# Kernel optimization log

Hardware: AMD Instinct MI355X
Metric: run time of the kernel (lower is better)

The kernel has to match this reference:

```python
import jax, jax.numpy as jnp
import numpy as np
import math

ANCHOR_SIZES = (128.0, 256.0, 512.0)
ANCHOR_RATIOS = (0.5, 1.0, 2.0)
NMS_THRESH = 0.7
PRE_NMS_TOPK = 6000   # rpn_test_prenms_topk (module is in eval at __init__)
POST_NMS_TOPK = 300   # rpn_test_topk
MIN_SIZE = 16.0
BBOX_CLIP = math.log(1000.0 / 16.0)


def _base_anchors():
    scales = jnp.array(ANCHOR_SIZES, jnp.float32)
    ratios = jnp.array(ANCHOR_RATIOS, jnp.float32)
    h_r = jnp.sqrt(ratios)
    w_r = 1.0 / h_r
    ws = (w_r[:, None] * scales[None, :]).reshape(-1)  # [A], ratio-major
    hs = (h_r[:, None] * scales[None, :]).reshape(-1)
    return jnp.stack([-ws, -hs, ws, hs], axis=1) * 0.5  # [A,4] centered at origin


def _grid_anchors(img_hw, feat_hw):
    Hi, Wi = img_hw
    Hf, Wf = feat_hw
    sy, sx = Hi // Hf, Wi // Wf  # feature stride
    shift_x = jnp.arange(Wf, dtype=jnp.float32) * sx
    shift_y = jnp.arange(Hf, dtype=jnp.float32) * sy
    yy, xx = jnp.meshgrid(shift_y, shift_x, indexing='ij')
    shifts = jnp.stack([xx, yy, xx, yy], axis=-1).reshape(-1, 1, 4)
    # layout (H, W, A) matches permute(0,2,3,1) flattening of the heads
    return (shifts + _base_anchors()[None]).reshape(-1, 4)


def _conv(x, w, b, pad):
    y = jax.lax.conv_general_dilated(x, w, (1, 1), pad,
                                     dimension_numbers=('NCHW', 'OIHW', 'NCHW'))
    return y + b[None, :, None, None]


def _decode(deltas, anchors):
    wa = anchors[:, 2] - anchors[:, 0]
    ha = anchors[:, 3] - anchors[:, 1]
    cxa = anchors[:, 0] + 0.5 * wa
    cya = anchors[:, 1] + 0.5 * ha
    dx, dy = deltas[:, 0], deltas[:, 1]
    dw = jnp.minimum(deltas[:, 2], BBOX_CLIP)
    dh = jnp.minimum(deltas[:, 3], BBOX_CLIP)
    cx = dx * wa + cxa
    cy = dy * ha + cya
    w = jnp.exp(dw) * wa
    h = jnp.exp(dh) * ha
    return jnp.stack([cx - 0.5 * w, cy - 0.5 * h, cx + 0.5 * w, cy + 0.5 * h], axis=1)


def _pairwise_iou(a, b):
    area_a = (a[:, 2] - a[:, 0]) * (a[:, 3] - a[:, 1])
    area_b = (b[:, 2] - b[:, 0]) * (b[:, 3] - b[:, 1])
    lt = jnp.maximum(a[:, None, :2], b[None, :, :2])
    rb = jnp.minimum(a[:, None, 2:], b[None, :, 2:])
    wh = jnp.clip(rb - lt, 0.0)
    inter = wh[..., 0] * wh[..., 1]
    return inter / (area_a[:, None] + area_b[None, :] - inter)


def _nms_keep(boxes, valid, thresh):
    # boxes are already sorted by descending score; greedy suppression
    N = boxes.shape[0]
    iou = _pairwise_iou(boxes, boxes)  # [N,N]
    idx = jnp.arange(N)

    def body(i, keep):
        sup = keep[i] & (iou[i] > thresh) & (idx > i)
        return keep & jnp.logical_not(sup)

    return jax.lax.fori_loop(0, N, body, valid)


def setup_inputs() -> dict:
    key = jax.random.key(0)
    ks = jax.random.split(key, 6)
    C, Hf, Wf = 1024, 100, 100
    Hi, Wi = 1600, 1600
    A = len(ANCHOR_SIZES) * len(ANCHOR_RATIOS)  # 9
    std = 0.01  # matches torch.nn.init.normal_(std=0.01), bias=0
    return {
        'input_image': jax.random.normal(ks[0], (1, 3, Hi, Wi), jnp.float32),
        'feature_map': jax.random.normal(ks[1], (1, C, Hf, Wf), jnp.float32),
        'conv_w': jax.random.normal(ks[2], (C, C, 3, 3), jnp.float32) * std,
        'conv_b': jnp.zeros((C,), jnp.float32),
        'obj_w': jax.random.normal(ks[3], (A, C, 1, 1), jnp.float32) * std,
        'obj_b': jnp.zeros((A,), jnp.float32),
        'reg_w': jax.random.normal(ks[4], (4 * A, C, 1, 1), jnp.float32) * std,
        'reg_b': jnp.zeros((4 * A,), jnp.float32),
    }


def reference(input_image, feature_map, conv_w, conv_b, obj_w, obj_b, reg_w, reg_b):
    Hi, Wi = input_image.shape[-2:]
    Hf, Wf = feature_map.shape[-2:]
    A = obj_w.shape[0]

    feats = jax.nn.relu(_conv(feature_map, conv_w, conv_b, 'SAME'))
    obj = _conv(feats, obj_w, obj_b, 'VALID')   # [N,A,Hf,Wf]
    reg = _conv(feats, reg_w, reg_b, 'VALID')   # [N,4A,Hf,Wf]

    obj_flat = jnp.transpose(obj, (0, 2, 3, 1)).reshape(-1)                 # [N*Hf*Wf*A]
    reg_flat = jnp.transpose(reg.reshape(-1, A, 4, Hf, Wf),
                             (0, 3, 4, 1, 2)).reshape(-1, 4)                # [N*Hf*Wf*A,4]

    anchors = _grid_anchors((Hi, Wi), (Hf, Wf))
    boxes = _decode(jax.lax.stop_gradient(reg_flat), anchors)
    probs = jax.nn.sigmoid(jax.lax.stop_gradient(obj_flat))

    k = min(PRE_NMS_TOPK, probs.shape[0])
    top_p, top_i = jax.lax.top_k(probs, k)
    b = boxes[top_i]
    b = jnp.stack([jnp.clip(b[:, 0], 0.0, Wi), jnp.clip(b[:, 1], 0.0, Hi),
                   jnp.clip(b[:, 2], 0.0, Wi), jnp.clip(b[:, 3], 0.0, Hi)], axis=1)
    valid = ((b[:, 2] - b[:, 0]) >= MIN_SIZE) & ((b[:, 3] - b[:, 1]) >= MIN_SIZE)

    keep = _nms_keep(b, valid, NMS_THRESH)
    masked = jnp.where(keep, top_p, -1.0)
    final_s, fi = jax.lax.top_k(masked, POST_NMS_TOPK)
    final_b = b[fi]
    good = final_s > 0.0  # zero-pad slots beyond the NMS survivor count
    proposals = jnp.where(good[:, None], final_b, 0.0)
    scores = jnp.where(good, final_s, 0.0)
    return proposals, scores
```

## Files before the change

### kernel.cpp

```cpp
#include <hip/hip_runtime.h>
#include <stdint.h>

typedef unsigned int uint32;
typedef unsigned long long uint64;

#define NPIX      10000
#define NCH       1024
#define NANCH     90000
#define PRE_TOPK  6000
#define POST_TOPK 300
#define SORT_N    8192
#define NWORDS    94
#define SUP_ROWS  6016
#define BBOX_CLIP_F 4.135166556742356f

#define TILE_H   8
#define TILE_W   16
#define HALO_H   10
#define HALO_W   18
#define HALO_WP  20
#define CICHUNK  16
#define CO_PER_WAVE 32

__device__ __forceinline__ uint64 shfl64(uint64 v, int lane) {
    int lo = __shfl((int)(uint32)v, lane);
    int hi = __shfl((int)(uint32)(v >> 32), lane);
    return ((uint64)(uint32)hi << 32) | (uint32)lo;
}

__global__ __launch_bounds__(256) void zero_out(float* __restrict__ out, int n) {
    int i = blockIdx.x * 256 + threadIdx.x;
    if (i < n) out[i] = 0.f;
}

__global__ __launch_bounds__(256) void repack_w(const float* __restrict__ w, float* __restrict__ W2) {
    int kk = blockIdx.x;
    int tile = blockIdx.y;
    int tci = (tile & 15) << 6;
    int tco = (tile >> 4) << 6;
    __shared__ float lds[64][65];
    int t = threadIdx.x;
    int c0 = t & 63;
    int r0 = t >> 6;
#pragma unroll
    for (int r = 0; r < 16; ++r) {
        int col = r0 + (r << 2);
        int ci = tci + c0;
        int co = tco + col;
        lds[col][c0] = w[((size_t)co * 1024 + ci) * 9 + kk];
    }
    __syncthreads();
#pragma unroll
    for (int r = 0; r < 16; ++r) {
        int row = r0 + (r << 2);
        int ci = tci + row;
        int co = tco + c0;
        W2[((size_t)kk * 1024 + ci) * 1024 + co] = lds[c0][row];
    }
}

__global__ __launch_bounds__(256) void conv_sw(const float* __restrict__ fm,
        const float* __restrict__ W2, const float* __restrict__ bias,
        float* __restrict__ feats) {
    __shared__ float xt[CICHUNK][HALO_H][HALO_WP];
    const int t = threadIdx.x;
    const int lane = t & 63;
    const int wv = t >> 6;
    const int tile = blockIdx.x;
    const int tx0 = (tile % 7) * TILE_W;
    const int ty0 = (tile / 7) * TILE_H;
    const int co0 = __builtin_amdgcn_readfirstlane((blockIdx.y << 7) + (wv << 5));
    const int ly = lane >> 3, lx = lane & 7;

    float acc0[CO_PER_WAVE] = {};
    float acc1[CO_PER_WAVE] = {};

#pragma unroll 1
    for (int c0 = 0; c0 < NCH; c0 += CICHUNK) {
        __syncthreads();
        for (int i = t; i < CICHUNK * HALO_H * HALO_W; i += 256) {
            int ci = i / (HALO_H * HALO_W);
            int rem = i - ci * (HALO_H * HALO_W);
            int hy = rem / HALO_W;
            int hx = rem - hy * HALO_W;
            int gy = ty0 - 1 + hy;
            int gx = tx0 - 1 + hx;
            bool ok = (gy >= 0) & (gy < 100) & (gx >= 0) & (gx < 100);
            xt[ci][hy][hx] = ok ? fm[(size_t)(c0 + ci) * NPIX + gy * 100 + gx] : 0.f;
        }
        __syncthreads();
#pragma unroll 1
        for (int ci = 0; ci < CICHUNK; ++ci) {
#pragma unroll
            for (int kk = 0; kk < 9; ++kk) {
                const int ky = kk / 3, kx2 = kk % 3;
                float x0v = xt[ci][ly + ky][lx + kx2];
                float x1v = xt[ci][ly + ky][lx + 8 + kx2];
                const float* wp = W2 + ((((size_t)kk << 10) + (size_t)(c0 + ci)) << 10) + co0;
#pragma unroll
                for (int c = 0; c < CO_PER_WAVE; ++c) {
                    float wgt = wp[c];
                    acc0[c] = fmaf(wgt, x0v, acc0[c]);
                    acc1[c] = fmaf(wgt, x1v, acc1[c]);
                }
            }
        }
    }

    const int gy = ty0 + ly;
    const int gx0 = tx0 + lx;
    const int gx1 = tx0 + 8 + lx;
    const bool oky = gy < 100;
#pragma unroll
    for (int c = 0; c < CO_PER_WAVE; ++c) {
        float b = bias[co0 + c];
        if (oky && (gx0 < 100)) feats[(size_t)(co0 + c) * NPIX + gy * 100 + gx0] = fmaxf(acc0[c] + b, 0.f);
        if (oky && (gx1 < 100)) feats[(size_t)(co0 + c) * NPIX + gy * 100 + gx1] = fmaxf(acc1[c] + b, 0.f);
    }
}

__global__ __launch_bounds__(256) void heads(const float* __restrict__ feats,
        const float* __restrict__ objw, const float* __restrict__ objb,
        const float* __restrict__ regw, const float* __restrict__ regb,
        uint32* __restrict__ keys32, float* __restrict__ regflat) {
    int p0 = blockIdx.x << 6;
    int t = threadIdx.x;
    int pl = t & 63;
    int g = t >> 6;
    __shared__ float fts[64][65];
    __shared__ float wl[48][64];
    float acc[12] = {};
    for (int c0 = 0; c0 < 1024; c0 += 64) {
        __syncthreads();
#pragma unroll
        for (int r = 0; r < 16; ++r) {
            int cc = g + (r << 2);
            int p = p0 + pl;
            fts[cc][pl] = (p < NPIX) ? feats[(size_t)(c0 + cc) * NPIX + p] : 0.f;
        }
#pragma unroll
        for (int i = 0; i < 12; ++i) {
            int flat = (i << 8) + t;
            int o = flat >> 6;
            int cc = flat & 63;
            float v = 0.f;
            if (o < 9) v = objw[o * 1024 + c0 + cc];
            else if (o < 45) v = regw[(o - 9) * 1024 + c0 + cc];
            wl[o][cc] = v;
        }
        __syncthreads();
#pragma unroll 16
        for (int cc = 0; cc < 64; ++cc) {
            float v = fts[cc][pl];
#pragma unroll
            for (int i = 0; i < 12; ++i)
                acc[i] = fmaf(v, wl[g + (i << 2)][cc], acc[i]);
        }
    }
    int p = p0 + pl;
    if (p < NPIX) {
#pragma unroll
        for (int i = 0; i < 12; ++i) {
            int o = g + (i << 2);
            if (o < 9) {
                float logit = acc[i] + objb[o];
                float prob = 1.f / (1.f + expf(-logit));
                keys32[p * 9 + o] = 0xFFFFFFFFu - __float_as_uint(prob);
            } else if (o < 45) {
                int ch = o - 9;
                float v = acc[i] + regb[ch];
                int a = ch >> 2, d = ch & 3;
                regflat[((size_t)p * 9 + a) * 4 + d] = v;
            }
        }
    }
}

__global__ __launch_bounds__(1024) void radix_select(const uint32* __restrict__ keys, uint32* __restrict__ meta) {
    __shared__ uint32 hist[256];
    __shared__ uint32 sPrefix, sK;
    int t = threadIdx.x;
    if (t == 0) { sPrefix = 0; sK = PRE_TOPK; }
    for (int pass = 0; pass < 4; ++pass) {
        int shift = 24 - pass * 8;
        uint32 kmask = pass ? (0xFFFFFFFFu << (32 - 8 * pass)) : 0u;
        if (t < 256) hist[t] = 0;
        __syncthreads();
        uint32 pref = sPrefix;
        for (int i = t; i < NANCH; i += 1024) {
            uint32 k = keys[i];
            if ((k & kmask) == pref) atomicAdd(&hist[(k >> shift) & 255], 1u);
        }
        __syncthreads();
        if (t == 0) {
            uint32 cum = 0, K = sK;
            for (int b = 0; b < 256; ++b) {
                uint32 c = hist[b];
                if (cum + c >= K) { sPrefix = pref | ((uint32)b << shift); sK = K - cum; break; }
                cum += c;
            }
        }
        __syncthreads();
    }
    if (t == 0) meta[0] = sPrefix;
}

__global__ __launch_bounds__(256) void compact_k(const uint32* __restrict__ keys, const uint32* __restrict__ meta,
        uint32* __restrict__ cnt, uint64* __restrict__ sel) {
    int i = blockIdx.x * 256 + threadIdx.x;
    if (i >= NANCH) return;
    uint32 T = meta[0];
    uint32 k = keys[i];
    if (k <= T) {
        uint32 pos = atomicAdd(cnt, 1u);
        if (pos < SORT_N) sel[pos] = ((uint64)k << 32) | (uint32)i;
    }
}

__global__ __launch_bounds__(1024) void bitonic_sort(const uint32* __restrict__ meta, const uint64* __restrict__ sel,
        uint64* __restrict__ sorted) {
    __shared__ uint64 arr[SORT_N];
    int t = threadIdx.x;
    uint32 cnt = meta[1]; if (cnt > SORT_N) cnt = SORT_N;
    for (int i = t; i < SORT_N; i += 1024) arr[i] = (i < (int)cnt) ? sel[i] : 0xFFFFFFFFFFFFFFFFull;
    __syncthreads();
    for (unsigned k = 2; k <= SORT_N; k <<= 1) {
        for (unsigned j = k >> 1; j > 0; j >>= 1) {
#pragma unroll 1
            for (int s = 0; s < SORT_N / 1024; ++s) {
                unsigned i = s * 1024 + t;
                unsigned l = i ^ j;
                if (l > i) {
                    uint64 a = arr[i], b = arr[l];
                    bool up = ((i & k) == 0);
                    if ((a > b) == up) { arr[i] = b; arr[l] = a; }
                }
            }
            __syncthreads();
        }
    }
    for (int i = t; i < PRE_TOPK; i += 1024) sorted[i] = arr[i];
}

__global__ __launch_bounds__(256) void decode_k(const uint64* __restrict__ sorted,
        const float* __restrict__ regflat,
        float4* __restrict__ boxes, float* __restrict__ probv, uint32* __restrict__ valid) {
    int i = blockIdx.x * 256 + threadIdx.x;
    if (i >= PRE_TOPK) return;
    uint64 v = sorted[i];
    uint32 idx = (uint32)v;
    uint32 key = (uint32)(v >> 32);
    float prob = __uint_as_float(0xFFFFFFFFu - key);
    int a = idx % 9;
    int p = idx / 9;
    int y = p / 100;
    int x = p - y * 100;
    const float ratios[3] = {0.5f, 1.0f, 2.0f};
    const float scales[3] = {128.f, 256.f, 512.f};
    float ratio = ratios[a / 3];
    float scale = scales[a % 3];
    float h_r = sqrtf(ratio);
    float w_r = 1.0f / h_r;
    float wsz = w_r * scale;
    float hsz = h_r * scale;
    float sx = 16.f * (float)x;
    float sy = 16.f * (float)y;
    float ax1 = sx - wsz * 0.5f;
    float ay1 = sy - hsz * 0.5f;
    float ax2 = sx + wsz * 0.5f;
    float ay2 = sy + hsz * 0.5f;
    float wa = ax2 - ax1;
    float ha = ay2 - ay1;
    float cxa = ax1 + 0.5f * wa;
    float cya = ay1 + 0.5f * ha;
    float dx = regflat[(size_t)idx * 4 + 0];
    float dy = regflat[(size_t)idx * 4 + 1];
    float dw = fminf(regflat[(size_t)idx * 4 + 2], BBOX_CLIP_F);
    float dh = fminf(regflat[(size_t)idx * 4 + 3], BBOX_CLIP_F);
    float cx = dx * wa + cxa;
    float cy = dy * ha + cya;
    float w = expf(dw) * wa;
    float h = expf(dh) * ha;
    float x1 = cx - 0.5f * w, y1 = cy - 0.5f * h, x2 = cx + 0.5f * w, y2 = cy + 0.5f * h;
    x1 = fminf(fmaxf(x1, 0.f), 1600.f);
    y1 = fminf(fmaxf(y1, 0.f), 1600.f);
    x2 = fminf(fmaxf(x2, 0.f), 1600.f);
    y2 = fminf(fmaxf(y2, 0.f), 1600.f);
    boxes[i] = make_float4(x1, y1, x2, y2);
    probv[i] = prob;
    valid[i] = (((x2 - x1) >= 16.f) & ((y2 - y1) >= 16.f)) ? 1u : 0u;
}

__global__ __launch_bounds__(64) void nms_pairs(const float4* __restrict__ boxes, uint64* __restrict__ sup) {
    int bi = blockIdx.y, bj = blockIdx.x;
    int t = threadIdx.x;
    int i = bi * 64 + t;
    if (bj < bi) { if (i < SUP_ROWS) sup[(size_t)i * NWORDS + bj] = 0; return; }
    __shared__ float4 bx[64];
    __shared__ float ab[64];
    int j0 = bj * 64;
    float4 bb = (j0 + t < PRE_TOPK) ? boxes[j0 + t] : make_float4(0, 0, 0, 0);
    bx[t] = bb;
    ab[t] = (bb.z - bb.x) * (bb.w - bb.y);
    __syncthreads();
    uint64 bits = 0;
    if (i < PRE_TOPK) {
        float4 ba = boxes[i];
        float aa = (ba.z - ba.x) * (ba.w - ba.y);
        for (int jj = 0; jj < 64; ++jj) {
            int j = j0 + jj;
            if (j > i && j < PRE_TOPK) {
                float4 bv = bx[jj];
                float ltx = fmaxf(ba.x, bv.x);
                float lty = fmaxf(ba.y, bv.y);
                float rbx = fminf(ba.z, bv.z);
                float rby = fminf(ba.w, bv.w);
                float wv = fmaxf(rbx - ltx, 0.f);
                float hv = fmaxf(rby - lty, 0.f);
                float inter = wv * hv;
                float iou = inter / (aa + ab[jj] - inter);
                if (iou > 0.7f) bits |= (1ull << jj);
            }
        }
    }
    if (i < SUP_ROWS) sup[(size_t)i * NWORDS + bj] = bits;
}

__global__ __launch_bounds__(64) void nms_scan(const uint32* __restrict__ valid, const uint64* __restrict__ sup,
        uint32* __restrict__ keeplist, uint32* __restrict__ kcount) {
    int l = threadIdx.x;
    __shared__ uint64 srow[64][95];
    uint64 r0 = 0, r1 = 0;
    for (int b = 0; b < 64; ++b) {
        int idx = l * 64 + b;
        if (idx < PRE_TOPK && valid[idx]) r0 |= (1ull << b);
    }
    if (l < NWORDS - 64) {
        int base = (64 + l) * 64;
        for (int b = 0; b < 64; ++b) {
            int idx = base + b;
            if (idx < PRE_TOPK && valid[idx]) r1 |= (1ull << b);
        }
    }
    int outc = 0;
    bool done = false;
    for (int c = 0; c < NWORDS && !done; ++c) {
        __syncthreads();
        for (int rr = 0; rr < 64; ++rr) {
            int row = c * 64 + rr;
            srow[rr][l] = sup[(size_t)row * NWORDS + l];
            if (l < NWORDS - 64) srow[rr][64 + l] = sup[(size_t)row * NWORDS + 64 + l];
        }
        __syncthreads();
        for (int ii = 0; ii < 64; ++ii) {
            int i = c * 64 + ii;
            if (i >= PRE_TOPK) break;
            uint64 kw = (c < 64) ? shfl64(r0, c) : shfl64(r1, c - 64);
            if ((kw >> ii) & 1ull) {
                if (l == 0) keeplist[outc] = (uint32)i;
                ++outc;
                if (outc >= POST_TOPK) { done = true; break; }
                r0 &= ~srow[ii][l];
                if (l < NWORDS - 64) r1 &= ~srow[ii][64 + l];
            }
        }
    }
    if (l == 0) *kcount = (uint32)outc;
}

__global__ __launch_bounds__(512) void finalize_k(const uint32* __restrict__ keeplist, const uint32* __restrict__ kcount,
        const float4* __restrict__ boxes, const float* __restrict__ probv, float* __restrict__ out) {
    int t = threadIdx.x;
    if (t < POST_TOPK) {
        uint32 kc = *kcount;
        if (t < (int)kc) {
            int i = keeplist[t];
            float4 b = boxes[i];
            out[t * 4 + 0] = b.x; out[t * 4 + 1] = b.y; out[t * 4 + 2] = b.z; out[t * 4 + 3] = b.w;
            out[1200 + t] = probv[i];
        } else {
            out[t * 4 + 0] = 0.f; out[t * 4 + 1] = 0.f; out[t * 4 + 2] = 0.f; out[t * 4 + 3] = 0.f;
            out[1200 + t] = 0.f;
        }
    }
}

extern "C" void kernel_launch(void* const* d_in, const int* in_sizes, int n_in,
                              void* d_out, int out_size, void* d_ws, size_t ws_size,
                              hipStream_t stream) {
    const float* fm = (const float*)d_in[1];
    const float* cw = (const float*)d_in[2];
    const float* cb = (const float*)d_in[3];
    const float* ow = (const float*)d_in[4];
    const float* ob = (const float*)d_in[5];
    const float* rw = (const float*)d_in[6];
    const float* rb = (const float*)d_in[7];
    float* out = (float*)d_out;

    uint8_t* base = (uint8_t*)d_ws;
    size_t off = 0;
    auto alloc = [&](size_t bytes) -> void* {
        void* p = base + off;
        off = (off + bytes + 255) & ~(size_t)255;
        return p;
    };
    float* feats    = (float*)alloc((size_t)NCH * NPIX * 4);
    uint32* meta    = (uint32*)alloc(64);
    uint32* keepl   = (uint32*)alloc(POST_TOPK * 4);
    uint32* kcount  = (uint32*)alloc(64);
    size_t ubase = off;
    float* W2       = (float*)alloc((size_t)9 * 1024 * 1024 * 4);
    size_t endA = off;
    off = ubase;
    uint32* keys    = (uint32*)alloc((size_t)NANCH * 4);
    float* regflat  = (float*)alloc((size_t)NANCH * 4 * 4);
    uint64* sel     = (uint64*)alloc((size_t)SORT_N * 8);
    uint64* sorted  = (uint64*)alloc((size_t)PRE_TOPK * 8);
    float4* boxes   = (float4*)alloc((size_t)PRE_TOPK * 16);
    float* probv    = (float*)alloc((size_t)PRE_TOPK * 4);
    uint32* validb  = (uint32*)alloc((size_t)PRE_TOPK * 4);
    uint64* sup     = (uint64*)alloc((size_t)SUP_ROWS * NWORDS * 8);
    size_t endB = off;
    size_t needed = (endA > endB) ? endA : endB;

    if (needed > ws_size) {
        zero_out<<<(out_size + 255) / 256, 256, 0, stream>>>(out, out_size);
        return;
    }

    hipMemsetAsync(meta, 0, 64, stream);

    repack_w<<<dim3(9, 256), 256, 0, stream>>>(cw, W2);
    conv_sw<<<dim3(91, 8), 256, 0, stream>>>(fm, W2, cb, feats);
    heads<<<157, 256, 0, stream>>>(feats, ow, ob, rw, rb, keys, regflat);
    radix_select<<<1, 1024, 0, stream>>>(keys, meta);
    compact_k<<<(NANCH + 255) / 256, 256, 0, stream>>>(keys, meta, meta + 1, sel);
    bitonic_sort<<<1, 1024, 0, stream>>>(meta, sel, sorted);
    decode_k<<<(PRE_TOPK + 255) / 256, 256, 0, stream>>>(sorted, regflat, boxes, probv, validb);
    nms_pairs<<<dim3(NWORDS, NWORDS), 64, 0, stream>>>(boxes, sup);
    nms_scan<<<1, 64, 0, stream>>>(validb, sup, keepl, kcount);
    finalize_k<<<1, 512, 0, stream>>>(keepl, kcount, boxes, probv, out);
}
```

Baseline: 3.707 ms.

## Repack conv weights per 16-channel tile and halve output channels per wave

Replaces the [kk][ci][co] weight repack with a [co-tile][ci][kk][16] layout, so each wave reads one contiguous 576-byte block of weights per input channel instead of nine strided 128-byte rows. Each wave now computes 16 output channels instead of 32, and the grid doubles along the output-channel axis. This cuts accumulator registers and may raise occupancy. In exchange the input halo tile loaded into shared memory is reused across half as many output channels, so shared-memory fills and global reads of the feature map double.

```diff
diff --git a/kernel.cpp b/kernel.cpp
--- a/kernel.cpp
+++ b/kernel.cpp
@@ -20,7 +20,7 @@
 #define HALO_W   18
 #define HALO_WP  20
 #define CICHUNK  16
-#define CO_PER_WAVE 32
+#define C_PER_WAVE 16
 
 __device__ __forceinline__ uint64 shfl64(uint64 v, int lane) {
     int lo = __shfl((int)(uint32)v, lane);
@@ -33,34 +33,26 @@
     if (i < n) out[i] = 0.f;
 }
 
-__global__ __launch_bounds__(256) void repack_w(const float* __restrict__ w, float* __restrict__ W2) {
-    int kk = blockIdx.x;
-    int tile = blockIdx.y;
-    int tci = (tile & 15) << 6;
-    int tco = (tile >> 4) << 6;
-    __shared__ float lds[64][65];
-    int t = threadIdx.x;
-    int c0 = t & 63;
-    int r0 = t >> 6;
-#pragma unroll
-    for (int r = 0; r < 16; ++r) {
-        int col = r0 + (r << 2);
-        int ci = tci + c0;
-        int co = tco + col;
-        lds[col][c0] = w[((size_t)co * 1024 + ci) * 9 + kk];
-    }
-    __syncthreads();
-#pragma unroll
-    for (int r = 0; r < 16; ++r) {
-        int row = r0 + (r << 2);
-        int ci = tci + row;
-        int co = tco + c0;
-        W2[((size_t)kk * 1024 + ci) * 1024 + co] = lds[c0][row];
-    }
-}
-
-__global__ __launch_bounds__(256) void conv_sw(const float* __restrict__ fm,
-        const float* __restrict__ W2, const float* __restrict__ bias,
+__global__ __launch_bounds__(256) void repack_w3(const float* __restrict__ w, float* __restrict__ W3) {
+    int cot = blockIdx.x;
+    int cib = blockIdx.y;
+    int t = threadIdx.x;
+    int c = t & 15;
+    int cil = t >> 4;
+    int ci = (cib << 6) | (cil << 2);
+    int co = (cot << 4) | c;
+#pragma unroll
+    for (int r = 0; r < 4; ++r) {
+        const float* src = w + ((size_t)co * 1024 + (ci + r)) * 9;
+        float* dst = W3 + (((size_t)cot * 1024 + (ci + r)) * 9) * 16 + c;
+#pragma unroll
+        for (int kk = 0; kk < 9; ++kk)
+            dst[kk * 16] = src[kk];
+    }
+}
+
+__global__ __launch_bounds__(256) void conv_sw2(const float* __restrict__ fm,
+        const float* __restrict__ W3, const float* __restrict__ bias,
         float* __restrict__ feats) {
     __shared__ float xt[CICHUNK][HALO_H][HALO_WP];
     const int t = threadIdx.x;
@@ -69,11 +61,12 @@
     const int tile = blockIdx.x;
     const int tx0 = (tile % 7) * TILE_W;
     const int ty0 = (tile / 7) * TILE_H;
-    const int co0 = __builtin_amdgcn_readfirstlane((blockIdx.y << 7) + (wv << 5));
+    const int cot = __builtin_amdgcn_readfirstlane((blockIdx.y << 2) + wv);
+    const int co0 = cot << 4;
     const int ly = lane >> 3, lx = lane & 7;
 
-    float acc0[CO_PER_WAVE] = {};
-    float acc1[CO_PER_WAVE] = {};
+    float acc0[C_PER_WAVE] = {};
+    float acc1[C_PER_WAVE] = {};
 
 #pragma unroll 1
     for (int c0 = 0; c0 < NCH; c0 += CICHUNK) {
@@ -91,15 +84,15 @@
         __syncthreads();
 #pragma unroll 1
         for (int ci = 0; ci < CICHUNK; ++ci) {
+            const float* wb = W3 + (((size_t)cot * 1024 + (size_t)(c0 + ci)) * 9) * 16;
 #pragma unroll
             for (int kk = 0; kk < 9; ++kk) {
                 const int ky = kk / 3, kx2 = kk % 3;
                 float x0v = xt[ci][ly + ky][lx + kx2];
                 float x1v = xt[ci][ly + ky][lx + 8 + kx2];
-                const float* wp = W2 + ((((size_t)kk << 10) + (size_t)(c0 + ci)) << 10) + co0;
-#pragma unroll
-                for (int c = 0; c < CO_PER_WAVE; ++c) {
-                    float wgt = wp[c];
+#pragma unroll
+                for (int c = 0; c < C_PER_WAVE; ++c) {
+                    float wgt = wb[kk * 16 + c];
                     acc0[c] = fmaf(wgt, x0v, acc0[c]);
                     acc1[c] = fmaf(wgt, x1v, acc1[c]);
                 }
@@ -112,7 +105,7 @@
     const int gx1 = tx0 + 8 + lx;
     const bool oky = gy < 100;
 #pragma unroll
-    for (int c = 0; c < CO_PER_WAVE; ++c) {
+    for (int c = 0; c < C_PER_WAVE; ++c) {
         float b = bias[co0 + c];
         if (oky && (gx0 < 100)) feats[(size_t)(co0 + c) * NPIX + gy * 100 + gx0] = fmaxf(acc0[c] + b, 0.f);
         if (oky && (gx1 < 100)) feats[(size_t)(co0 + c) * NPIX + gy * 100 + gx1] = fmaxf(acc1[c] + b, 0.f);
@@ -409,7 +402,7 @@
     uint32* keepl   = (uint32*)alloc(POST_TOPK * 4);
     uint32* kcount  = (uint32*)alloc(64);
     size_t ubase = off;
-    float* W2       = (float*)alloc((size_t)9 * 1024 * 1024 * 4);
+    float* W3       = (float*)alloc((size_t)64 * 1024 * 9 * 16 * 4);
     size_t endA = off;
     off = ubase;
     uint32* keys    = (uint32*)alloc((size_t)NANCH * 4);
@@ -430,8 +423,8 @@
 
     hipMemsetAsync(meta, 0, 64, stream);
 
-    repack_w<<<dim3(9, 256), 256, 0, stream>>>(cw, W2);
-    conv_sw<<<dim3(91, 8), 256, 0, stream>>>(fm, W2, cb, feats);
+    repack_w3<<<dim3(64, 16), 256, 0, stream>>>(cw, W3);
+    conv_sw2<<<dim3(91, 16), 256, 0, stream>>>(fm, W3, cb, feats);
     heads<<<157, 256, 0, stream>>>(feats, ow, ob, rw, rb, keys, regflat);
     radix_select<<<1, 1024, 0, stream>>>(keys, meta);
     compact_k<<<(NANCH + 255) / 256, 256, 0, stream>>>(keys, meta, meta + 1, sel);
```

Measured after the change: 3.361 ms. -9.3%, faster.
